# Performance work log

Measured on AMD Instinct MI355X. Metric: run time of the kernel, lower is better.

## Reference

```python
import jax, jax.numpy as jnp
import numpy as np

DIM = 768
NUM_HEADS = 12
HEAD_DIM = DIM // NUM_HEADS


def setup_inputs() -> dict:
    key = jax.random.key(0)
    k1, k2, k3 = jax.random.split(key, 3)
    B, N = 2, 2048
    x = jax.random.normal(k1, (B, N, DIM), dtype=jnp.float32)
    qkv_w = jax.random.normal(k2, (3 * DIM, DIM), dtype=jnp.float32) * 0.02
    proj_w = jax.random.normal(k3, (DIM, DIM), dtype=jnp.float32) * 0.02
    proj_b = jnp.zeros((DIM,), dtype=jnp.float32)
    freq_params = jnp.ones((NUM_HEADS, 1), dtype=jnp.float32) * 0.5  # Parameter init ones*0.5
    return {"x": x, "qkv_w": qkv_w, "proj_w": proj_w, "proj_b": proj_b,
            "freq_params": freq_params}


def _forward(x, qkv_w, proj_w, proj_b, freq_params):
    B, N, C = x.shape
    H, D = NUM_HEADS, HEAD_DIM
    scale = D ** (-0.5)
    # qkv projection -> (3, B, H, N, D)
    qkv = (x @ qkv_w.T).reshape(B, N, 3, H, D).transpose(2, 0, 3, 1, 4)
    q, k, v = qkv[0], qkv[1], qkv[2]
    # FFT along the token axis (axis=2 of [B,H,N,D])
    q_freq = jnp.fft.fft(q, axis=2)
    k_freq = jnp.fft.fft(k, axis=2)
    # Adaptive per-head low-pass: cutoff = int(N * sigmoid(freq_param)),
    # frequencies >= cutoff attenuated by exp(-(i - cutoff) / (N/4)).
    cutoff = jnp.floor(N * jax.nn.sigmoid(freq_params[:, 0]))        # (H,)
    idx = jnp.arange(N, dtype=jnp.float32)                            # (N,)
    rel = idx[None, :] - cutoff[:, None]                              # (H, N)
    atten = jnp.where(rel >= 0, jnp.exp(-rel / (N / 4.0)), 1.0)       # (H, N)
    atten = atten[None, :, :, None]                                   # (1, H, N, 1)
    q_filt = jnp.fft.ifft(q_freq * atten, axis=2).real
    k_filt = jnp.fft.ifft(k_freq * atten, axis=2).real
    # Attention
    attn = jnp.einsum('bhnd,bhmd->bhnm', q_filt, k_filt) * scale
    attn = jax.nn.softmax(attn, axis=-1)
    out = jnp.einsum('bhnm,bhmd->bhnd', attn, v)
    out = out.transpose(0, 2, 1, 3).reshape(B, N, C)
    return out @ proj_w.T + proj_b


def reference(x, qkv_w, proj_w, proj_b, freq_params):
    return _forward(x, qkv_w, proj_w, proj_b, freq_params)
```

## Files before the change

### kernel.cpp

```cpp
#include <hip/hip_runtime.h>
#include <math.h>

#define SEQ 2048
#define NH 12
#define HD 64
#define DIM 768

typedef _Float16 half_t;
typedef _Float16 f16x8 __attribute__((ext_vector_type(8)));
typedef _Float16 f16x4 __attribute__((ext_vector_type(4)));
typedef float f32x4 __attribute__((ext_vector_type(4)));

__device__ __forceinline__ void dma16(const half_t* g, half_t* l) {
  __builtin_amdgcn_global_load_lds(
      (const __attribute__((address_space(1))) unsigned int*)g,
      (__attribute__((address_space(3))) unsigned int*)l, 16, 0, 0);
}

__global__ __launch_bounds__(256) void cvt_f32_f16(
    const float* __restrict__ a, const float* __restrict__ b,
    const float* __restrict__ c, half_t* __restrict__ a16,
    half_t* __restrict__ b16, half_t* __restrict__ c16) {
  const size_t NA = 786432, NB = 442368;
  size_t i = (size_t)blockIdx.x * 256 + threadIdx.x;
  const float* src; half_t* dst; size_t off;
  if (i < NA) { src = a; dst = a16; off = i; }
  else if (i < NA + NB) { src = b; dst = b16; off = i - NA; }
  else { src = c; dst = c16; off = i - NA - NB; }
  float4 v = *(const float4*)&src[off * 4];
  f16x4 h;
  h[0] = (half_t)v.x; h[1] = (half_t)v.y; h[2] = (half_t)v.z; h[3] = (half_t)v.w;
  *(f16x4*)&dst[off * 4] = h;
}

__global__ __launch_bounds__(256) void gemm_qkv_f16(
    const half_t* __restrict__ x, const half_t* __restrict__ w,
    float* __restrict__ qT, float* __restrict__ kT, half_t* __restrict__ vb) {
  __shared__ half_t As[128][64];
  __shared__ half_t Bs[128][64];
  const int tid = threadIdx.x;
  const int lane = tid & 63, wave = tid >> 6;
  const int quad = lane >> 4, l16 = lane & 15;
  const int wr = wave >> 1, wc = wave & 1;
  const int row0 = blockIdx.y * 128;
  const int col0 = blockIdx.x * 128;
  const int srow = tid >> 3;
  const int schk = tid & 7;

  f32x4 acc[4][4] = {};

  for (int k0 = 0; k0 < DIM; k0 += 64) {
    f16x8 av[4], bv[4];
#pragma unroll
    for (int p = 0; p < 4; p++) {
      av[p] = *(const f16x8*)&x[(size_t)(row0 + srow + p * 32) * DIM + k0 + schk * 8];
      bv[p] = *(const f16x8*)&w[(size_t)(col0 + srow + p * 32) * DIM + k0 + schk * 8];
    }
    __syncthreads();
#pragma unroll
    for (int p = 0; p < 4; p++) {
      int r = srow + p * 32;
      int cs = ((schk ^ (r & 7)) << 3);
      *(f16x8*)&As[r][cs] = av[p];
      *(f16x8*)&Bs[r][cs] = bv[p];
    }
    __syncthreads();
#pragma unroll
    for (int ks = 0; ks < 2; ks++) {
      f16x8 af[4], bf[4];
#pragma unroll
      for (int i = 0; i < 4; i++) {
        int rr = wr * 64 + i * 16 + l16;
        af[i] = *(const f16x8*)&As[rr][((ks * 4 + quad) ^ (rr & 7)) << 3];
      }
#pragma unroll
      for (int j = 0; j < 4; j++) {
        int rr = wc * 64 + j * 16 + l16;
        bf[j] = *(const f16x8*)&Bs[rr][((ks * 4 + quad) ^ (rr & 7)) << 3];
      }
#pragma unroll
      for (int i = 0; i < 4; i++)
#pragma unroll
        for (int j = 0; j < 4; j++)
          acc[i][j] = __builtin_amdgcn_mfma_f32_16x16x32_f16(af[i], bf[j], acc[i][j], 0, 0, 0);
    }
  }

  const int fbase = col0 + wc * 64;
#pragma unroll
  for (int i = 0; i < 4; i++) {
    int n = row0 + wr * 64 + i * 16 + quad * 4;
    int b = n >> 11, nn = n & (SEQ - 1);
#pragma unroll
    for (int j = 0; j < 4; j++) {
      int f = fbase + j * 16 + l16;
      if (col0 < 1536) {
        float* dst = (col0 < 768) ? qT : kT;
        int fo = (col0 < 768) ? f : f - 768;
        *(f32x4*)&dst[((size_t)(b * 768 + fo)) * SEQ + nn] = acc[i][j];
      } else {
        int fo = f - 1536;
        int h = fo >> 6, d = fo & 63;
        int bh = b * NH + h;
        int ch = nn >> 6, cw = (nn & 63) >> 3, sub = nn & 7;
        f16x4 hv;
#pragma unroll
        for (int r = 0; r < 4; r++) hv[r] = (half_t)acc[i][j][r];
        *(f16x4*)&vb[((((size_t)bh * 32 + ch) * 64 + d) << 6) +
                     (((cw ^ (d & 7)) << 3) + sub)] = hv;
      }
    }
  }
}

__device__ __forceinline__ void bitrev_via_tmp(float* a, float* tmp, int tid) {
  for (int n = tid; n < SEQ; n += 256) {
    int r = (int)(__brev((unsigned)n) >> 21);
    tmp[r + (r >> 5)] = a[n];
  }
  __syncthreads();
  for (int n = tid; n < SEQ; n += 256) a[n] = tmp[n + (n >> 5)];
  __syncthreads();
}

__device__ __forceinline__ void fft2048_r4(float* re, float* im, float* tmp,
                                           int tid, float dir) {
  bitrev_via_tmp(re, tmp, tid);
  bitrev_via_tmp(im, tmp, tid);
  for (int L = 2; L <= 512; L <<= 2) {
    const int h = L >> 1;
    const float ang = dir * 3.14159265358979f / (float)L;
#pragma unroll 2
    for (int g = tid; g < SEQ / 4; g += 256) {
      int p = g & (h - 1);
      int i0 = ((g & ~(h - 1)) << 2) | p;
      float s2, c2;
      __sincosf(ang * (float)p, &s2, &c2);
      float c1 = c2 * c2 - s2 * s2, s1 = 2.0f * c2 * s2;
      float ar = re[i0],         ai = im[i0];
      float br = re[i0 + h],     bi = im[i0 + h];
      float cr = re[i0 + L],     ci = im[i0 + L];
      float dr = re[i0 + L + h], di = im[i0 + L + h];
      float t1r = c1 * br - s1 * bi, t1i = c1 * bi + s1 * br;
      float a1r = ar + t1r, a1i = ai + t1i;
      float b1r = ar - t1r, b1i = ai - t1i;
      float t2r = c1 * dr - s1 * di, t2i = c1 * di + s1 * dr;
      float e1r = cr + t2r, e1i = ci + t2i;
      float d1r = cr - t2r, d1i = ci - t2i;
      float ur = c2 * e1r - s2 * e1i, ui = c2 * e1i + s2 * e1r;
      float vr = c2 * d1r - s2 * d1i, vi = c2 * d1i + s2 * d1r;
      float wr = -dir * vi, wi = dir * vr;
      re[i0]         = a1r + ur; im[i0]         = a1i + ui;
      re[i0 + L]     = a1r - ur; im[i0 + L]     = a1i - ui;
      re[i0 + h]     = b1r + wr; im[i0 + h]     = b1i + wi;
      re[i0 + L + h] = b1r - wr; im[i0 + L + h] = b1i - wi;
    }
    __syncthreads();
  }
  {
    const float ang = dir * 6.283185307179586f / 2048.0f;
#pragma unroll 2
    for (int j = tid; j < 1024; j += 256) {
      float s, c;
      __sincosf(ang * (float)j, &s, &c);
      float x0r = re[j], x0i = im[j], x1r = re[j + 1024], x1i = im[j + 1024];
      float tr = c * x1r - s * x1i, ti = c * x1i + s * x1r;
      re[j] = x0r + tr;        im[j] = x0i + ti;
      re[j + 1024] = x0r - tr; im[j + 1024] = x0i - ti;
    }
    __syncthreads();
  }
}

__global__ __launch_bounds__(256) void fft_filter(
    const float* __restrict__ qT, const float* __restrict__ kT,
    half_t* __restrict__ qh, half_t* __restrict__ kh,
    const float* __restrict__ freq_params) {
  __shared__ float re[SEQ];
  __shared__ float im[SEQ];
  __shared__ float tmp[2112];
  const int tid = threadIdx.x;
  const int idx = blockIdx.x;
  const int h = (idx >> 6) % NH;
  const float* qrow = qT + (size_t)idx * SEQ;
  const float* krow = kT + (size_t)idx * SEQ;

  for (int n = tid; n < SEQ; n += 256) { re[n] = qrow[n]; im[n] = krow[n]; }
  __syncthreads();
  fft2048_r4(re, im, tmp, tid, -1.0f);

  const float fp = freq_params[h];
  const float sig = 1.0f / (1.0f + expf(-fp));
  const float cutoff = floorf((float)SEQ * sig);

  for (int n = tid; n <= SEQ / 2; n += 256) {
    int m = (SEQ - n) & (SEQ - 1);
    float ar = re[n], ai = im[n], br = re[m], bi = im[m];
    float Qnr = 0.5f * (ar + br), Qni = 0.5f * (ai - bi);
    float Knr = 0.5f * (ai + bi), Kni = 0.5f * (br - ar);
    float Qmr = 0.5f * (br + ar), Qmi = 0.5f * (bi - ai);
    float Kmr = 0.5f * (bi + ai), Kmi = 0.5f * (ar - br);
    float reln = (float)n - cutoff;
    float relm = (float)m - cutoff;
    float An = (reln >= 0.0f) ? expf(-reln * (1.0f / 512.0f)) : 1.0f;
    float Am = (relm >= 0.0f) ? expf(-relm * (1.0f / 512.0f)) : 1.0f;
    float fQnr = An * Qnr, fQni = An * Qni, fKnr = An * Knr, fKni = An * Kni;
    float fQmr = Am * Qmr, fQmi = Am * Qmi, fKmr = Am * Kmr, fKmi = Am * Kmi;
    float Qsr = 0.5f * (fQnr + fQmr), Qsi = 0.5f * (fQni - fQmi);
    float Ksr = 0.5f * (fKnr + fKmr), Ksi = 0.5f * (fKni - fKmi);
    re[n] = Qsr - Ksi; im[n] = Qsi + Ksr;
    float Qsr2 = 0.5f * (fQmr + fQnr), Qsi2 = 0.5f * (fQmi - fQni);
    float Ksr2 = 0.5f * (fKmr + fKnr), Ksi2 = 0.5f * (fKmi - fKni);
    re[m] = Qsr2 - Ksi2; im[m] = Qsi2 + Ksr2;
  }
  __syncthreads();
  fft2048_r4(re, im, tmp, tid, +1.0f);

  const float inv = 1.0f / (float)SEQ;
  half_t* qo = qh + (size_t)idx * SEQ;
  half_t* ko = kh + (size_t)idx * SEQ;
  for (int n = tid; n < SEQ; n += 256) {
    qo[n] = (half_t)(re[n] * inv);
    ko[n] = (half_t)(im[n] * inv);
  }
}

__global__ __launch_bounds__(256) void transpose_qk16(
    const half_t* __restrict__ qh, const half_t* __restrict__ kh,
    half_t* __restrict__ qA, half_t* __restrict__ kA) {
  __shared__ half_t tl[64][65];
  const int swz = blockIdx.z;
  const half_t* src = swz ? kh : qh;
  half_t* dst = swz ? kA : qA;
  const int t = threadIdx.x;
  const int N0 = blockIdx.x * 64;
  const int bh = blockIdx.y;
#pragma unroll
  for (int i = 0; i < 2; i++) {
    int idx = i * 256 + t;
    int d = idx >> 3, n8 = (idx & 7) << 3;
    f16x8 v = *(const f16x8*)&src[((size_t)(bh * 64 + d)) * SEQ + N0 + n8];
#pragma unroll
    for (int j = 0; j < 8; j++) tl[d][n8 + j] = v[j];
  }
  __syncthreads();
#pragma unroll
  for (int i = 0; i < 2; i++) {
    int idx = i * 256 + t;
    int nl = idx >> 3, chunk = idx & 7;
    f16x8 v;
#pragma unroll
    for (int j = 0; j < 8; j++) v[j] = tl[chunk * 8 + j][nl];
    int cs = swz ? (chunk ^ (nl & 7)) : chunk;
    *(f16x8*)&dst[((size_t)(bh * SEQ + N0 + nl)) * 64 + cs * 8] = v;
  }
}

__global__ __launch_bounds__(256) void attention_v5(
    const half_t* __restrict__ qA, const half_t* __restrict__ kA,
    const half_t* __restrict__ vb, float* __restrict__ part0,
    float* __restrict__ part1, float* __restrict__ Lp0,
    float* __restrict__ Lp1) {
  __shared__ half_t ks[2][64][64];
  __shared__ half_t vs[64][64];
  const int t = threadIdx.x;
  const int lane = t & 63, wave = t >> 6;
  const int quad = lane >> 4, l16 = lane & 15;
  const int id = blockIdx.x;
  const int bh = (id & 7) * 3 + ((id >> 3) % 3);
  const int rest = id / 24;
  const int qt = rest >> 1, mh = rest & 1;
  const int N0 = qt * 128;
  float* part = mh ? part1 : part0;
  float* Lp = mh ? Lp1 : Lp0;
  const half_t* kbase = kA + ((size_t)bh * SEQ + mh * 1024) * 64;
  const half_t* vbase = vb + (((size_t)bh * 32 + mh * 16) << 12);

  f16x8 qlo[2], qhi[2];
#pragma unroll
  for (int u = 0; u < 2; u++) {
    int n = N0 + wave * 32 + u * 16 + l16;
    const half_t* qp = qA + ((size_t)bh * SEQ + n) * 64;
    qlo[u] = *(const f16x8*)(qp + quad * 8);
    qhi[u] = *(const f16x8*)(qp + 32 + quad * 8);
  }

#pragma unroll
  for (int i = 0; i < 2; i++) {
    int ins = wave * 2 + i;
    dma16(kbase + ins * 512 + lane * 8, &ks[0][ins * 8][0]);
  }
  __syncthreads();

  f32x4 acc[2][4] = {};
  float Ls[2] = {0.0f, 0.0f};
  const float SC = 0.18033688011112042f;
  const float SH = -2.8853900817779268f;

  for (int c = 0; c < 16; c++) {
    const int cur = c & 1;
    const half_t* vsrc = vbase + ((size_t)c << 12);
#pragma unroll
    for (int i = 0; i < 2; i++) {
      int ins = wave * 2 + i;
      dma16(vsrc + ins * 512 + lane * 8, &vs[ins * 8][0]);
    }
    const int cn = (c < 15) ? c + 1 : 0;
#pragma unroll
    for (int i = 0; i < 2; i++) {
      int ins = wave * 2 + i;
      dma16(kbase + (size_t)cn * 4096 + ins * 512 + lane * 8,
            &ks[1 - cur][ins * 8][0]);
    }

    f16x4 pf[2][4];
#pragma unroll
    for (int j = 0; j < 4; j++) {
      int row = j * 16 + l16;
      int sw = row & 7;
      f16x8 klo = *(const f16x8*)&ks[cur][row][(quad ^ sw) * 8];
      f16x8 khi = *(const f16x8*)&ks[cur][row][((quad + 4) ^ sw) * 8];
#pragma unroll
      for (int u = 0; u < 2; u++) {
        f32x4 s = {};
        s = __builtin_amdgcn_mfma_f32_16x16x32_f16(klo, qlo[u], s, 0, 0, 0);
        s = __builtin_amdgcn_mfma_f32_16x16x32_f16(khi, qhi[u], s, 0, 0, 0);
#pragma unroll
        for (int r = 0; r < 4; r++) {
          float p = exp2f(fmaf(s[r], SC, SH));
          Ls[u] += p;
          pf[u][j][r] = (half_t)p;
        }
      }
    }
    __syncthreads();

#pragma unroll
    for (int j = 0; j < 4; j++)
#pragma unroll
      for (int dt = 0; dt < 4; dt++) {
        int d = dt * 16 + l16;
        int cc = ((2 * j + (quad >> 1)) ^ (d & 7));
        f16x4 bv = *(const f16x4*)&vs[d][cc * 8 + (quad & 1) * 4];
        acc[0][dt] = __builtin_amdgcn_mfma_f32_16x16x16f16(pf[0][j], bv, acc[0][dt], 0, 0, 0);
        acc[1][dt] = __builtin_amdgcn_mfma_f32_16x16x16f16(pf[1][j], bv, acc[1][dt], 0, 0, 0);
      }
    __syncthreads();
  }

#pragma unroll
  for (int u = 0; u < 2; u++) {
    float L = Ls[u];
    L += __shfl_xor(L, 16, 64);
    L += __shfl_xor(L, 32, 64);
    if (quad == 0) Lp[(size_t)bh * SEQ + N0 + wave * 32 + u * 16 + l16] = L;
#pragma unroll
    for (int dt = 0; dt < 4; dt++) {
#pragma unroll
      for (int r = 0; r < 4; r++) {
        int n = N0 + wave * 32 + u * 16 + quad * 4 + r;
        part[((size_t)bh * SEQ + n) * 64 + dt * 16 + l16] = acc[u][dt][r];
      }
    }
  }
}

__global__ __launch_bounds__(256) void combine_o(
    const float* __restrict__ p0, const float* __restrict__ p1,
    const float* __restrict__ L0, const float* __restrict__ L1,
    half_t* __restrict__ ao) {
  int idx = blockIdx.x * 256 + threadIdx.x;
  int row = idx >> 4;
  int d = (idx & 15) << 2;
  f32x4 a = *(const f32x4*)&p0[(size_t)row * 64 + d];
  f32x4 b = *(const f32x4*)&p1[(size_t)row * 64 + d];
  float inv = 1.0f / (L0[row] + L1[row]);
  int bh = row >> 11, n = row & (SEQ - 1);
  int bb = bh / NH, h = bh % NH;
  f16x4 o;
#pragma unroll
  for (int r = 0; r < 4; r++) o[r] = (half_t)((a[r] + b[r]) * inv);
  *(f16x4*)&ao[((size_t)(bb * SEQ + n)) * DIM + h * 64 + d] = o;
}

__global__ __launch_bounds__(256) void gemm_proj_f16(
    const half_t* __restrict__ ao, const half_t* __restrict__ w,
    const float* __restrict__ bias, float* __restrict__ out) {
  __shared__ half_t As[128][64];
  __shared__ half_t Bs[128][64];
  const int tid = threadIdx.x;
  const int lane = tid & 63, wave = tid >> 6;
  const int quad = lane >> 4, l16 = lane & 15;
  const int wr = wave >> 1, wc = wave & 1;
  const int row0 = blockIdx.y * 128;
  const int col0 = blockIdx.x * 128;
  const int srow = tid >> 3;
  const int schk = tid & 7;

  f32x4 acc[4][4] = {};

  for (int k0 = 0; k0 < DIM; k0 += 64) {
    f16x8 av[4], bv[4];
#pragma unroll
    for (int p = 0; p < 4; p++) {
      av[p] = *(const f16x8*)&ao[(size_t)(row0 + srow + p * 32) * DIM + k0 + schk * 8];
      bv[p] = *(const f16x8*)&w[(size_t)(col0 + srow + p * 32) * DIM + k0 + schk * 8];
    }
    __syncthreads();
#pragma unroll
    for (int p = 0; p < 4; p++) {
      int r = srow + p * 32;
      int cs = ((schk ^ (r & 7)) << 3);
      *(f16x8*)&As[r][cs] = av[p];
      *(f16x8*)&Bs[r][cs] = bv[p];
    }
    __syncthreads();
#pragma unroll
    for (int ks = 0; ks < 2; ks++) {
      f16x8 af[4], bf[4];
#pragma unroll
      for (int i = 0; i < 4; i++) {
        int rr = wr * 64 + i * 16 + l16;
        af[i] = *(const f16x8*)&As[rr][((ks * 4 + quad) ^ (rr & 7)) << 3];
      }
#pragma unroll
      for (int j = 0; j < 4; j++) {
        int rr = wc * 64 + j * 16 + l16;
        bf[j] = *(const f16x8*)&Bs[rr][((ks * 4 + quad) ^ (rr & 7)) << 3];
      }
#pragma unroll
      for (int i = 0; i < 4; i++)
#pragma unroll
        for (int j = 0; j < 4; j++)
          acc[i][j] = __builtin_amdgcn_mfma_f32_16x16x32_f16(af[i], bf[j], acc[i][j], 0, 0, 0);
    }
  }

#pragma unroll
  for (int i = 0; i < 4; i++) {
    int m = row0 + wr * 64 + i * 16 + quad * 4;
#pragma unroll
    for (int j = 0; j < 4; j++) {
      int f = col0 + wc * 64 + j * 16 + l16;
      float bj = bias[f];
#pragma unroll
      for (int r = 0; r < 4; r++)
        out[(size_t)(m + r) * DIM + f] = acc[i][j][r] + bj;
    }
  }
}

extern "C" void kernel_launch(void* const* d_in, const int* in_sizes, int n_in,
                              void* d_out, int out_size, void* d_ws, size_t ws_size,
                              hipStream_t stream) {
  (void)in_sizes; (void)n_in; (void)out_size; (void)ws_size;
  const float* x      = (const float*)d_in[0];
  const float* qkv_w  = (const float*)d_in[1];
  const float* proj_w = (const float*)d_in[2];
  const float* proj_b = (const float*)d_in[3];
  const float* freq   = (const float*)d_in[4];
  float* out = (float*)d_out;
  char* ws = (char*)d_ws;

  half_t* wp16 = (half_t*)(ws);
  float*  qT   = (float*)(ws + 1179648);
  float*  kT   = (float*)(ws + 13762560);
  half_t* v_b  = (half_t*)(ws + 26345472);
  half_t* x16  = (half_t*)(ws + 32636928);
  half_t* w16  = (half_t*)(ws + 38928384);
  half_t* q_h  = (half_t*)(ws + 42467328);
  half_t* k_h  = (half_t*)(ws + 32636928);
  float*  part0 = (float*)(ws + 1179648);
  float*  part1 = (float*)(ws + 13762560);
  float*  Lp0  = (float*)(ws + 38928384);
  float*  Lp1  = (float*)(ws + 38928384 + 196608);
  half_t* ao   = (half_t*)(ws + 42467328);
  half_t* qA   = (half_t*)d_out;
  half_t* kA   = (half_t*)((char*)d_out + 6291456);

  cvt_f32_f16<<<5376, 256, 0, stream>>>(x, qkv_w, proj_w, x16, w16, wp16);
  gemm_qkv_f16<<<dim3(18, 32), 256, 0, stream>>>(x16, w16, qT, kT, v_b);
  fft_filter<<<1536, 256, 0, stream>>>(qT, kT, q_h, k_h, freq);
  transpose_qk16<<<dim3(32, 24, 2), 256, 0, stream>>>(q_h, k_h, qA, kA);
  attention_v5<<<768, 256, 0, stream>>>(qA, kA, v_b, part0, part1, Lp0, Lp1);
  combine_o<<<3072, 256, 0, stream>>>(part0, part1, Lp0, Lp1, ao);
  gemm_proj_f16<<<dim3(6, 32), 256, 0, stream>>>(ao, wp16, proj_b, out);
}
```

Measured before the change: 218.8 us.

## Use DIF forward/DIT inverse FFT to skip bit reversal; double-buffer V in attention

The forward FFT becomes a decimation-in-frequency radix-4 pass that leaves its output in bit-reversed order, and the inverse stays decimation-in-time and consumes bit-reversed input. This removes both bit-reversal permutations and the tmp shared buffer. The Hermitian split/recombine filter step is replaced by one real symmetric gain 0.5*(A(n)+A(N-n)) applied at the bit-reversed index, using fast __expf. In attention, V tiles are now double-buffered like K and prefetched one chunk ahead, cutting the two barriers per iteration to one, at the cost of more LDS.

```diff
diff --git a/kernel.cpp b/kernel.cpp
--- a/kernel.cpp
+++ b/kernel.cpp
@@ -113,23 +113,52 @@
   }
 }
 
-__device__ __forceinline__ void bitrev_via_tmp(float* a, float* tmp, int tid) {
-  for (int n = tid; n < SEQ; n += 256) {
-    int r = (int)(__brev((unsigned)n) >> 21);
-    tmp[r + (r >> 5)] = a[n];
+__device__ __forceinline__ void fft2048_dif_fwd(float* re, float* im, int tid) {
+  for (int M = 2048; M >= 8; M >>= 2) {
+    const int q = M >> 2;
+    const float ang = -6.283185307179586f / (float)M;
+#pragma unroll 2
+    for (int g = tid; g < 512; g += 256) {
+      int j = g & (q - 1);
+      int base = ((g & ~(q - 1)) << 2) | j;
+      float s1, c1;
+      __sincosf(ang * (float)j, &s1, &c1);
+      float c2 = c1 * c1 - s1 * s1, s2 = 2.0f * c1 * s1;
+      float Ar = re[base],         Ai = im[base];
+      float Br = re[base + q],     Bi = im[base + q];
+      float Cr = re[base + 2*q],   Ci = im[base + 2*q];
+      float Dr = re[base + 3*q],   Di = im[base + 3*q];
+      float A1r = Ar + Cr, A1i = Ai + Ci;
+      float t1r = Ar - Cr, t1i = Ai - Ci;
+      float C1r = c1 * t1r - s1 * t1i, C1i = c1 * t1i + s1 * t1r;
+      float B1r = Br + Dr, B1i = Bi + Di;
+      float t2r = Br - Dr, t2i = Bi - Di;
+      float u2r = c1 * t2r - s1 * t2i, u2i = c1 * t2i + s1 * t2r;
+      float D1r = u2i, D1i = -u2r;
+      re[base]         = A1r + B1r; im[base]         = A1i + B1i;
+      float t3r = A1r - B1r, t3i = A1i - B1i;
+      re[base + q]     = c2 * t3r - s2 * t3i;
+      im[base + q]     = c2 * t3i + s2 * t3r;
+      re[base + 2*q]   = C1r + D1r; im[base + 2*q]   = C1i + D1i;
+      float t4r = C1r - D1r, t4i = C1i - D1i;
+      re[base + 3*q]   = c2 * t4r - s2 * t4i;
+      im[base + 3*q]   = c2 * t4i + s2 * t4r;
+    }
+    __syncthreads();
+  }
+#pragma unroll 2
+  for (int i = tid; i < 1024; i += 256) {
+    float ar = re[2*i], ai = im[2*i], br = re[2*i+1], bi = im[2*i+1];
+    re[2*i]   = ar + br; im[2*i]   = ai + bi;
+    re[2*i+1] = ar - br; im[2*i+1] = ai - bi;
   }
   __syncthreads();
-  for (int n = tid; n < SEQ; n += 256) a[n] = tmp[n + (n >> 5)];
-  __syncthreads();
-}
-
-__device__ __forceinline__ void fft2048_r4(float* re, float* im, float* tmp,
-                                           int tid, float dir) {
-  bitrev_via_tmp(re, tmp, tid);
-  bitrev_via_tmp(im, tmp, tid);
+}
+
+__device__ __forceinline__ void fft2048_dit_inv(float* re, float* im, int tid) {
   for (int L = 2; L <= 512; L <<= 2) {
     const int h = L >> 1;
-    const float ang = dir * 3.14159265358979f / (float)L;
+    const float ang = 3.14159265358979f / (float)L;
 #pragma unroll 2
     for (int g = tid; g < SEQ / 4; g += 256) {
       int p = g & (h - 1);
@@ -149,7 +178,7 @@
       float d1r = cr - t2r, d1i = ci - t2i;
       float ur = c2 * e1r - s2 * e1i, ui = c2 * e1i + s2 * e1r;
       float vr = c2 * d1r - s2 * d1i, vi = c2 * d1i + s2 * d1r;
-      float wr = -dir * vi, wi = dir * vr;
+      float wr = -vi, wi = vr;
       re[i0]         = a1r + ur; im[i0]         = a1i + ui;
       re[i0 + L]     = a1r - ur; im[i0 + L]     = a1i - ui;
       re[i0 + h]     = b1r + wr; im[i0 + h]     = b1i + wi;
@@ -158,7 +187,7 @@
     __syncthreads();
   }
   {
-    const float ang = dir * 6.283185307179586f / 2048.0f;
+    const float ang = 6.283185307179586f / 2048.0f;
 #pragma unroll 2
     for (int j = tid; j < 1024; j += 256) {
       float s, c;
@@ -178,7 +207,6 @@
     const float* __restrict__ freq_params) {
   __shared__ float re[SEQ];
   __shared__ float im[SEQ];
-  __shared__ float tmp[2112];
   const int tid = threadIdx.x;
   const int idx = blockIdx.x;
   const int h = (idx >> 6) % NH;
@@ -187,34 +215,26 @@
 
   for (int n = tid; n < SEQ; n += 256) { re[n] = qrow[n]; im[n] = krow[n]; }
   __syncthreads();
-  fft2048_r4(re, im, tmp, tid, -1.0f);
+  fft2048_dif_fwd(re, im, tid);
 
   const float fp = freq_params[h];
   const float sig = 1.0f / (1.0f + expf(-fp));
   const float cutoff = floorf((float)SEQ * sig);
 
-  for (int n = tid; n <= SEQ / 2; n += 256) {
+#pragma unroll 2
+  for (int p = tid; p < SEQ; p += 256) {
+    int n = (int)(__brev((unsigned)p) >> 21);
     int m = (SEQ - n) & (SEQ - 1);
-    float ar = re[n], ai = im[n], br = re[m], bi = im[m];
-    float Qnr = 0.5f * (ar + br), Qni = 0.5f * (ai - bi);
-    float Knr = 0.5f * (ai + bi), Kni = 0.5f * (br - ar);
-    float Qmr = 0.5f * (br + ar), Qmi = 0.5f * (bi - ai);
-    float Kmr = 0.5f * (bi + ai), Kmi = 0.5f * (ar - br);
-    float reln = (float)n - cutoff;
-    float relm = (float)m - cutoff;
-    float An = (reln >= 0.0f) ? expf(-reln * (1.0f / 512.0f)) : 1.0f;
-    float Am = (relm >= 0.0f) ? expf(-relm * (1.0f / 512.0f)) : 1.0f;
-    float fQnr = An * Qnr, fQni = An * Qni, fKnr = An * Knr, fKni = An * Kni;
-    float fQmr = Am * Qmr, fQmi = Am * Qmi, fKmr = Am * Kmr, fKmi = Am * Kmi;
-    float Qsr = 0.5f * (fQnr + fQmr), Qsi = 0.5f * (fQni - fQmi);
-    float Ksr = 0.5f * (fKnr + fKmr), Ksi = 0.5f * (fKni - fKmi);
-    re[n] = Qsr - Ksi; im[n] = Qsi + Ksr;
-    float Qsr2 = 0.5f * (fQmr + fQnr), Qsi2 = 0.5f * (fQmi - fQni);
-    float Ksr2 = 0.5f * (fKmr + fKnr), Ksi2 = 0.5f * (fKmi - fKni);
-    re[m] = Qsr2 - Ksi2; im[m] = Qsi2 + Ksr2;
+    float r1 = (float)n - cutoff;
+    float r2 = (float)m - cutoff;
+    float A1 = (r1 >= 0.0f) ? __expf(-r1 * (1.0f / 512.0f)) : 1.0f;
+    float A2 = (r2 >= 0.0f) ? __expf(-r2 * (1.0f / 512.0f)) : 1.0f;
+    float Ae = 0.5f * (A1 + A2);
+    re[p] *= Ae; im[p] *= Ae;
   }
   __syncthreads();
-  fft2048_r4(re, im, tmp, tid, +1.0f);
+
+  fft2048_dit_inv(re, im, tid);
 
   const float inv = 1.0f / (float)SEQ;
   half_t* qo = qh + (size_t)idx * SEQ;
@@ -256,13 +276,13 @@
   }
 }
 
-__global__ __launch_bounds__(256) void attention_v5(
+__global__ __launch_bounds__(256) void attention_v6(
     const half_t* __restrict__ qA, const half_t* __restrict__ kA,
     const half_t* __restrict__ vb, float* __restrict__ part0,
     float* __restrict__ part1, float* __restrict__ Lp0,
     float* __restrict__ Lp1) {
   __shared__ half_t ks[2][64][64];
-  __shared__ half_t vs[64][64];
+  __shared__ half_t vs[2][64][64];
   const int t = threadIdx.x;
   const int lane = t & 63, wave = t >> 6;
   const int quad = lane >> 4, l16 = lane & 15;
@@ -289,8 +309,8 @@
   for (int i = 0; i < 2; i++) {
     int ins = wave * 2 + i;
     dma16(kbase + ins * 512 + lane * 8, &ks[0][ins * 8][0]);
-  }
-  __syncthreads();
+    dma16(vbase + ins * 512 + lane * 8, &vs[0][ins * 8][0]);
+  }
 
   f32x4 acc[2][4] = {};
   float Ls[2] = {0.0f, 0.0f};
@@ -299,18 +319,16 @@
 
   for (int c = 0; c < 16; c++) {
     const int cur = c & 1;
-    const half_t* vsrc = vbase + ((size_t)c << 12);
-#pragma unroll
-    for (int i = 0; i < 2; i++) {
-      int ins = wave * 2 + i;
-      dma16(vsrc + ins * 512 + lane * 8, &vs[ins * 8][0]);
-    }
+    __syncthreads();
+
     const int cn = (c < 15) ? c + 1 : 0;
 #pragma unroll
     for (int i = 0; i < 2; i++) {
       int ins = wave * 2 + i;
       dma16(kbase + (size_t)cn * 4096 + ins * 512 + lane * 8,
             &ks[1 - cur][ins * 8][0]);
+      dma16(vbase + (size_t)cn * 4096 + ins * 512 + lane * 8,
+            &vs[1 - cur][ins * 8][0]);
     }
 
     f16x4 pf[2][4];
@@ -333,7 +351,6 @@
         }
       }
     }
-    __syncthreads();
 
 #pragma unroll
     for (int j = 0; j < 4; j++)
@@ -341,11 +358,10 @@
       for (int dt = 0; dt < 4; dt++) {
         int d = dt * 16 + l16;
         int cc = ((2 * j + (quad >> 1)) ^ (d & 7));
-        f16x4 bv = *(const f16x4*)&vs[d][cc * 8 + (quad & 1) * 4];
+        f16x4 bv = *(const f16x4*)&vs[cur][d][cc * 8 + (quad & 1) * 4];
         acc[0][dt] = __builtin_amdgcn_mfma_f32_16x16x16f16(pf[0][j], bv, acc[0][dt], 0, 0, 0);
         acc[1][dt] = __builtin_amdgcn_mfma_f32_16x16x16f16(pf[1][j], bv, acc[1][dt], 0, 0, 0);
       }
-    __syncthreads();
   }
 
 #pragma unroll
@@ -482,7 +498,7 @@
   gemm_qkv_f16<<<dim3(18, 32), 256, 0, stream>>>(x16, w16, qT, kT, v_b);
   fft_filter<<<1536, 256, 0, stream>>>(qT, kT, q_h, k_h, freq);
   transpose_qk16<<<dim3(32, 24, 2), 256, 0, stream>>>(q_h, k_h, qA, kA);
-  attention_v5<<<768, 256, 0, stream>>>(qA, kA, v_b, part0, part1, Lp0, Lp1);
+  attention_v6<<<768, 256, 0, stream>>>(qA, kA, v_b, part0, part1, Lp0, Lp1);
   combine_o<<<3072, 256, 0, stream>>>(part0, part1, Lp0, Lp1, ao);
   gemm_proj_f16<<<dim3(6, 32), 256, 0, stream>>>(ao, wp16, proj_b, out);
 }
```

After: 216.2 us. Within noise of the previous version (-1.2%).
